# Optimization experiments

Hardware: AMD Instinct MI355X
Metric: run time of the kernel (lower is better)

Reference implementation:

```python
import jax, jax.numpy as jnp
import numpy as np
from jax import lax

B, H, W, CIN = 16, 224, 224, 8
F = 256            # filter_inpt feature dim
K = 3              # ksize (square)
NC = 16            # n_channels (output channels)
NP = CIN * NC * K * K  # 1152 dynamic filter params per sample


def setup_inputs() -> dict:
    key = jax.random.key(0)
    ks = jax.random.split(key, 8)
    s_in = 1.0 / np.sqrt(F)
    return {
        "inpt": jax.random.normal(ks[0], (B, H, W, CIN), jnp.float32),
        "filter_inpt": jax.random.normal(ks[1], (B, F), jnp.float32),
        # param_layer_1 (ELU affine, F -> F)
        "W1": jax.random.normal(ks[2], (F, F), jnp.float32) * s_in,
        "b1": jnp.zeros((F,), jnp.float32),
        # dynamic_weights affine (F -> NP), uniform_unit_scaling(0.1)-like scale
        "Wd": jax.random.normal(ks[3], (F, NP), jnp.float32) * (0.1 * s_in),
        "bd": jnp.zeros((NP,), jnp.float32),
        # dynamic_bias affine (F -> NC), scale sqrt(2)
        "Wb": jax.random.normal(ks[4], (F, NC), jnp.float32) * (np.sqrt(2.0) * s_in),
        "bb": jnp.zeros((NC,), jnp.float32),
        # static learned bias (1,1,1,NC)
        "dfn_bias": jax.random.normal(ks[5], (1, 1, 1, NC), jnp.float32) * 0.01,
    }


def reference(inpt, filter_inpt, W1, b1, Wd, bd, Wb, bb, dfn_bias):
    # param layers: (n_param_layers - 1) = 1 ELU affine keeping width F
    h = jax.nn.elu(filter_inpt @ W1 + b1)                      # [B, F]
    dyn = h @ Wd + bd                                          # [B, CIN*NC*K*K]
    # per-sample filter, ordered (Cin, kh, kw, out_ch) to match patch layout below
    w = dyn.reshape(B, CIN * K * K, NC)                        # [B, P, NC]
    # im2col patches: conv_general_dilated_patches on NCHW -> [B, CIN*K*K, H, W]
    patches = lax.conv_general_dilated_patches(
        jnp.transpose(inpt, (0, 3, 1, 2)), (K, K), (1, 1), 'SAME')
    patches = jnp.transpose(patches, (0, 2, 3, 1))             # [B, H, W, P]
    out = jnp.einsum('bhwp,bpc->bhwc', patches, w)             # [B, H, W, NC]
    # adaptive (per-sample) bias + static bias
    out = out + (h @ Wb + bb)[:, None, None, :] + dfn_bias
    return jax.nn.elu(out)
```

## Files before the change

### kernel.cpp

```cpp
#include <hip/hip_runtime.h>
#include <math.h>

constexpr int BN  = 16;
constexpr int HH  = 224;
constexpr int WW  = 224;
constexpr int CI  = 8;
constexpr int FF  = 256;
constexpr int NC  = 16;
constexpr int NP  = 1152;

typedef __attribute__((ext_vector_type(8))) short short8;
typedef __attribute__((ext_vector_type(4))) float f32x4;

__device__ __forceinline__ float elu_f(float x) {
    return x > 0.0f ? x : (__expf(x) - 1.0f);
}

__device__ __forceinline__ void split8(const float* v, short8& hi, short8& lo) {
#pragma unroll
    for (int j = 0; j < 8; ++j) {
        const unsigned u = __float_as_uint(v[j]);
        hi[j] = (short)(u >> 16);
        const float hf = __uint_as_float(u & 0xffff0000u);
        lo[j] = (short)(__float_as_uint(v[j] - hf) >> 16);
    }
}

__global__ __launch_bounds__(128) void k_h(const float* __restrict__ fi,
                                           const float* __restrict__ W1,
                                           const float* __restrict__ b1,
                                           const float* __restrict__ bd,
                                           const float* __restrict__ bb,
                                           const float* __restrict__ dfn,
                                           float* __restrict__ h_out,
                                           float* __restrict__ w_out,
                                           float* __restrict__ bias_out) {
    __shared__ float x[FF];
    int bid = blockIdx.x;
    int b = bid >> 1, half = bid & 1;
    int t = threadIdx.x;
    x[t]       = fi[b * FF + t];
    x[t + 128] = fi[b * FF + t + 128];
    __syncthreads();
    int col = half * 128 + t;
    float acc = b1[col];
#pragma unroll 8
    for (int k = 0; k < FF; ++k) acc = fmaf(x[k], W1[k * FF + col], acc);
    h_out[b * FF + col] = elu_f(acc);

    const int gid = bid * 128 + t;
    for (int i = gid; i < BN * NP; i += 4096) {
        const int c = i - (i / NP) * NP;
        w_out[i] = bd[c];
    }
    if (gid < BN * NC) bias_out[gid] = bb[gid & 15] + dfn[gid & 15];
}

__global__ __launch_bounds__(128) void k_dyn(const float* __restrict__ h_in,
                                             const float* __restrict__ Wd,
                                             const float* __restrict__ Wb,
                                             float* __restrict__ w_out,
                                             float* __restrict__ bias_out) {
    __shared__ float hs[16][32];
    const int bid = blockIdx.x;
    const int cg  = bid % 9;
    const int ks  = bid / 9;
    const int k0  = ks * 32;
    const int t   = threadIdx.x;

#pragma unroll
    for (int j = 0; j < 4; ++j) {
        const int idx = t + 128 * j;
        const int bi = idx >> 5, kk = idx & 31;
        hs[bi][kk] = h_in[bi * FF + k0 + kk];
    }
    __syncthreads();

    const int i = cg * 128 + t;
    float a[16];
#pragma unroll
    for (int b = 0; b < 16; ++b) a[b] = 0.0f;

#pragma unroll 8
    for (int kk = 0; kk < 32; ++kk) {
        const float w = Wd[(size_t)(k0 + kk) * NP + i];
#pragma unroll
        for (int b = 0; b < 16; ++b) a[b] = fmaf(hs[b][kk], w, a[b]);
    }
#pragma unroll
    for (int b = 0; b < 16; ++b) atomicAdd(&w_out[b * NP + i], a[b]);

    if (cg == 0) {
#pragma unroll
        for (int r = 0; r < 2; ++r) {
            const int p = t + r * 128;
            const int b = p >> 4, c = p & 15;
            float s = 0.0f;
#pragma unroll 8
            for (int kk = 0; kk < 32; ++kk)
                s = fmaf(hs[b][kk], Wb[(size_t)(k0 + kk) * NC + c], s);
            atomicAdd(&bias_out[b * NC + c], s);
        }
    }
}

__global__ __launch_bounds__(128) void k_conv(const float* __restrict__ in,
                                              const float* __restrict__ w_all,
                                              const float* __restrict__ bias_all,
                                              float* __restrict__ out) {
    const int b    = blockIdx.z;
    const int half = blockIdx.x;
    const int t    = threadIdx.x;
    const int wid  = t >> 6;
    const int lane = t & 63;
    const int cl   = lane & 15;
    const int g    = lane >> 4;
    const int y    = blockIdx.y * 2 + wid;

    int  dyL[3], dxL[3];
    bool real[3];
#pragma unroll
    for (int c = 0; c < 3; ++c) {
        const int tap = c * 4 + g;
        real[c] = (tap < 9);
        const int tp = real[c] ? tap : 0;
        dyL[c] = tp / 3;
        dxL[c] = tp - 3 * dyL[c];
    }

    const float* __restrict__ wq = w_all + b * NP;
    short8 bhi0, blo0, bhi1, blo1, bhi2, blo2;
    {
        float wv[8];
#pragma unroll
        for (int i = 0; i < 8; ++i)
            wv[i] = real[0] ? wq[(i * 9 + (0 * 4 + g)) * NC + cl] : 0.0f;
        split8(wv, bhi0, blo0);
#pragma unroll
        for (int i = 0; i < 8; ++i)
            wv[i] = real[1] ? wq[(i * 9 + (1 * 4 + g)) * NC + cl] : 0.0f;
        split8(wv, bhi1, blo1);
#pragma unroll
        for (int i = 0; i < 8; ++i)
            wv[i] = real[2] ? wq[(i * 9 + (2 * 4 + g)) * NC + cl] : 0.0f;
        split8(wv, bhi2, blo2);
    }

    size_t ro[3];
    bool   okr[3];
#pragma unroll
    for (int c = 0; c < 3; ++c) {
        const int iy = y + dyL[c] - 1;
        okr[c] = real[c] && ((unsigned)iy < (unsigned)HH);
        const int iyc = min(max(iy, 0), HH - 1);
        ro[c] = ((size_t)(b * HH + iyc) * WW) * CI;
    }

    const float bias = bias_all[b * NC + cl];
    const size_t orow = ((size_t)(b * HH + y) * WW) * NC;

#pragma unroll 1
    for (int tx = 0; tx < 7; ++tx) {
        const int x0 = (half * 7 + tx) * 16;
        f32x4 accM = {bias, bias, bias, bias};
        f32x4 accC = {0.f, 0.f, 0.f, 0.f};

#pragma unroll
        for (int c = 0; c < 3; ++c) {
            const int  ix = x0 + cl + dxL[c] - 1;
            const bool ok = okr[c] && ((unsigned)ix < (unsigned)WW);
            const int  ixc = min(max(ix, 0), WW - 1);
            const float4* pp = (const float4*)(in + ro[c] + (size_t)ixc * CI);
            const float4 a0 = pp[0];
            const float4 a1 = pp[1];
            float av[8];
            av[0] = ok ? a0.x : 0.0f;
            av[1] = ok ? a0.y : 0.0f;
            av[2] = ok ? a0.z : 0.0f;
            av[3] = ok ? a0.w : 0.0f;
            av[4] = ok ? a1.x : 0.0f;
            av[5] = ok ? a1.y : 0.0f;
            av[6] = ok ? a1.z : 0.0f;
            av[7] = ok ? a1.w : 0.0f;
            short8 ahi, alo;
            split8(av, ahi, alo);
            const short8 bh = (c == 0) ? bhi0 : (c == 1) ? bhi1 : bhi2;
            const short8 bl = (c == 0) ? blo0 : (c == 1) ? blo1 : blo2;
            accM = __builtin_amdgcn_mfma_f32_16x16x32_bf16(ahi, bh, accM, 0, 0, 0);
            accC = __builtin_amdgcn_mfma_f32_16x16x32_bf16(alo, bh, accC, 0, 0, 0);
            accC = __builtin_amdgcn_mfma_f32_16x16x32_bf16(ahi, bl, accC, 0, 0, 0);
        }

#pragma unroll
        for (int r = 0; r < 4; ++r) {
            const int px = g * 4 + r;
            out[orow + (size_t)(x0 + px) * NC + cl] = elu_f(accM[r] + accC[r]);
        }
    }
}

extern "C" void kernel_launch(void* const* d_in, const int* in_sizes, int n_in,
                              void* d_out, int out_size, void* d_ws, size_t ws_size,
                              hipStream_t stream) {
    const float* inpt = (const float*)d_in[0];
    const float* fi   = (const float*)d_in[1];
    const float* W1   = (const float*)d_in[2];
    const float* b1   = (const float*)d_in[3];
    const float* Wd   = (const float*)d_in[4];
    const float* bd   = (const float*)d_in[5];
    const float* Wb   = (const float*)d_in[6];
    const float* bb   = (const float*)d_in[7];
    const float* dfn  = (const float*)d_in[8];
    float* out = (float*)d_out;

    float* ws    = (float*)d_ws;
    float* h     = ws;
    float* wDyn  = ws + 4096;
    float* biasA = ws + 4096 + 18432;

    k_h  <<<32, 128, 0, stream>>>(fi, W1, b1, bd, bb, dfn, h, wDyn, biasA);
    k_dyn<<<72, 128, 0, stream>>>(h, Wd, Wb, wDyn, biasA);
    k_conv<<<dim3(2, 112, BN), 128, 0, stream>>>(inpt, wDyn, biasA, out);
}
```

Measured before the change: 45.88 us.

## Fuse hidden-layer GEMV into dynamic-weight kernel and fold biases into conv

Removes the separate k_h kernel. Each k_dynf block now recomputes its 32-wide slice of the ELU hidden layer for all samples, using a shared-memory copy of filter_inpt. The bd/bb/dfn bias initialisation moves into the conv kernel's weight and bias loads, and the accumulators are zeroed with a memset instead. The lo/hi correction MFMAs are also split into independent accumulators to break the dependency chain. The trade is redundant W1 reads across the 9 column-group blocks, plus an extra memset node in place of a kernel launch.

```diff
diff --git a/kernel.cpp b/kernel.cpp
--- a/kernel.cpp
+++ b/kernel.cpp
@@ -26,42 +26,15 @@
     }
 }
 
-__global__ __launch_bounds__(128) void k_h(const float* __restrict__ fi,
-                                           const float* __restrict__ W1,
-                                           const float* __restrict__ b1,
-                                           const float* __restrict__ bd,
-                                           const float* __restrict__ bb,
-                                           const float* __restrict__ dfn,
-                                           float* __restrict__ h_out,
-                                           float* __restrict__ w_out,
-                                           float* __restrict__ bias_out) {
-    __shared__ float x[FF];
-    int bid = blockIdx.x;
-    int b = bid >> 1, half = bid & 1;
-    int t = threadIdx.x;
-    x[t]       = fi[b * FF + t];
-    x[t + 128] = fi[b * FF + t + 128];
-    __syncthreads();
-    int col = half * 128 + t;
-    float acc = b1[col];
-#pragma unroll 8
-    for (int k = 0; k < FF; ++k) acc = fmaf(x[k], W1[k * FF + col], acc);
-    h_out[b * FF + col] = elu_f(acc);
-
-    const int gid = bid * 128 + t;
-    for (int i = gid; i < BN * NP; i += 4096) {
-        const int c = i - (i / NP) * NP;
-        w_out[i] = bd[c];
-    }
-    if (gid < BN * NC) bias_out[gid] = bb[gid & 15] + dfn[gid & 15];
-}
-
-__global__ __launch_bounds__(128) void k_dyn(const float* __restrict__ h_in,
-                                             const float* __restrict__ Wd,
-                                             const float* __restrict__ Wb,
-                                             float* __restrict__ w_out,
-                                             float* __restrict__ bias_out) {
-    __shared__ float hs[16][32];
+__global__ __launch_bounds__(128) void k_dynf(const float* __restrict__ fi,
+                                              const float* __restrict__ W1,
+                                              const float* __restrict__ b1,
+                                              const float* __restrict__ Wd,
+                                              const float* __restrict__ Wb,
+                                              float* __restrict__ w_out,
+                                              float* __restrict__ bias_out) {
+    __shared__ float fis[BN][FF];
+    __shared__ float hs[BN][32];
     const int bid = blockIdx.x;
     const int cg  = bid % 9;
     const int ks  = bid / 9;
@@ -69,10 +42,26 @@
     const int t   = threadIdx.x;
 
 #pragma unroll
-    for (int j = 0; j < 4; ++j) {
-        const int idx = t + 128 * j;
-        const int bi = idx >> 5, kk = idx & 31;
-        hs[bi][kk] = h_in[bi * FF + k0 + kk];
+    for (int e = 0; e < 8; ++e) {
+        const int q = e * 128 + t;
+        ((float4*)fis)[q] = ((const float4*)fi)[q];
+    }
+    __syncthreads();
+
+    {
+        const int kk = t & 31, rg = t >> 5;
+        float hacc[4];
+#pragma unroll
+        for (int r = 0; r < 4; ++r) hacc[r] = b1[k0 + kk];
+#pragma unroll 8
+        for (int j = 0; j < FF; ++j) {
+            const float w1 = W1[j * FF + k0 + kk];
+#pragma unroll
+            for (int r = 0; r < 4; ++r)
+                hacc[r] = fmaf(fis[rg * 4 + r][j], w1, hacc[r]);
+        }
+#pragma unroll
+        for (int r = 0; r < 4; ++r) hs[rg * 4 + r][kk] = elu_f(hacc[r]);
     }
     __syncthreads();
 
@@ -107,6 +96,9 @@
 __global__ __launch_bounds__(128) void k_conv(const float* __restrict__ in,
                                               const float* __restrict__ w_all,
                                               const float* __restrict__ bias_all,
+                                              const float* __restrict__ bd,
+                                              const float* __restrict__ bb,
+                                              const float* __restrict__ dfn,
                                               float* __restrict__ out) {
     const int b    = blockIdx.z;
     const int half = blockIdx.x;
@@ -133,16 +125,22 @@
     {
         float wv[8];
 #pragma unroll
-        for (int i = 0; i < 8; ++i)
-            wv[i] = real[0] ? wq[(i * 9 + (0 * 4 + g)) * NC + cl] : 0.0f;
+        for (int i = 0; i < 8; ++i) {
+            const int idx = (i * 9 + (0 * 4 + g)) * NC + cl;
+            wv[i] = real[0] ? (wq[idx] + bd[idx]) : 0.0f;
+        }
         split8(wv, bhi0, blo0);
 #pragma unroll
-        for (int i = 0; i < 8; ++i)
-            wv[i] = real[1] ? wq[(i * 9 + (1 * 4 + g)) * NC + cl] : 0.0f;
+        for (int i = 0; i < 8; ++i) {
+            const int idx = (i * 9 + (1 * 4 + g)) * NC + cl;
+            wv[i] = real[1] ? (wq[idx] + bd[idx]) : 0.0f;
+        }
         split8(wv, bhi1, blo1);
 #pragma unroll
-        for (int i = 0; i < 8; ++i)
-            wv[i] = real[2] ? wq[(i * 9 + (2 * 4 + g)) * NC + cl] : 0.0f;
+        for (int i = 0; i < 8; ++i) {
+            const int idx = (i * 9 + (2 * 4 + g)) * NC + cl;
+            wv[i] = real[2] ? (wq[idx] + bd[idx]) : 0.0f;
+        }
         split8(wv, bhi2, blo2);
     }
 
@@ -156,14 +154,15 @@
         ro[c] = ((size_t)(b * HH + iyc) * WW) * CI;
     }
 
-    const float bias = bias_all[b * NC + cl];
+    const float bias = bias_all[b * NC + cl] + bb[cl] + dfn[cl];
     const size_t orow = ((size_t)(b * HH + y) * WW) * NC;
 
 #pragma unroll 1
     for (int tx = 0; tx < 7; ++tx) {
         const int x0 = (half * 7 + tx) * 16;
         f32x4 accM = {bias, bias, bias, bias};
-        f32x4 accC = {0.f, 0.f, 0.f, 0.f};
+        f32x4 accL = {0.f, 0.f, 0.f, 0.f};
+        f32x4 accH = {0.f, 0.f, 0.f, 0.f};
 
 #pragma unroll
         for (int c = 0; c < 3; ++c) {
@@ -187,14 +186,15 @@
             const short8 bh = (c == 0) ? bhi0 : (c == 1) ? bhi1 : bhi2;
             const short8 bl = (c == 0) ? blo0 : (c == 1) ? blo1 : blo2;
             accM = __builtin_amdgcn_mfma_f32_16x16x32_bf16(ahi, bh, accM, 0, 0, 0);
-            accC = __builtin_amdgcn_mfma_f32_16x16x32_bf16(alo, bh, accC, 0, 0, 0);
-            accC = __builtin_amdgcn_mfma_f32_16x16x32_bf16(ahi, bl, accC, 0, 0, 0);
+            accL = __builtin_amdgcn_mfma_f32_16x16x32_bf16(alo, bh, accL, 0, 0, 0);
+            accH = __builtin_amdgcn_mfma_f32_16x16x32_bf16(ahi, bl, accH, 0, 0, 0);
         }
 
 #pragma unroll
         for (int r = 0; r < 4; ++r) {
             const int px = g * 4 + r;
-            out[orow + (size_t)(x0 + px) * NC + cl] = elu_f(accM[r] + accC[r]);
+            out[orow + (size_t)(x0 + px) * NC + cl] =
+                elu_f(accM[r] + accL[r] + accH[r]);
         }
     }
 }
@@ -214,11 +214,12 @@
     float* out = (float*)d_out;
 
     float* ws    = (float*)d_ws;
-    float* h     = ws;
     float* wDyn  = ws + 4096;
     float* biasA = ws + 4096 + 18432;
 
-    k_h  <<<32, 128, 0, stream>>>(fi, W1, b1, bd, bb, dfn, h, wDyn, biasA);
-    k_dyn<<<72, 128, 0, stream>>>(h, Wd, Wb, wDyn, biasA);
-    k_conv<<<dim3(2, 112, BN), 128, 0, stream>>>(inpt, wDyn, biasA, out);
-}
+    hipMemsetAsync(wDyn, 0, (size_t)(BN * NP + BN * NC) * sizeof(float), stream);
+
+    k_dynf<<<72, 128, 0, stream>>>(fi, W1, b1, Wd, Wb, wDyn, biasA);
+    k_conv<<<dim3(2, 112, BN), 128, 0, stream>>>(inpt, wDyn, biasA,
+                                                 bd, bb, dfn, out);
+}
```

After: 59.69 us. 1.3x slower.
